# Optimization experiments

Hardware: AMD Instinct MI355X
Metric: run time of the kernel (lower is better)

## Reference

```python
import jax, jax.numpy as jnp
import numpy as np

B, L, D = 2, 2048, 2048
H, G, HD = 16, 4, 128
EPS = 1e-6
THETA_BASE = 10000.0


def setup_inputs() -> dict:
    key = jax.random.key(0)
    ks = jax.random.split(key, 5)
    x = jax.random.normal(ks[0], (B, L, D), jnp.float32)
    Wq = jax.random.normal(ks[1], (D, H * HD), jnp.float32) * 0.02
    Wk = jax.random.normal(ks[2], (D, G * HD), jnp.float32) * 0.02
    Wv = jax.random.normal(ks[3], (D, G * HD), jnp.float32) * 0.02
    Wo = jax.random.normal(ks[4], (H * HD, D), jnp.float32) * 0.02
    q_scale = jnp.ones((HD,), jnp.float32)
    k_scale = jnp.ones((HD,), jnp.float32)
    # Well-formed RoPE tables of shape [L, HD] (duplicated-half layout expected by apply_rope)
    inv_freq = 1.0 / (THETA_BASE ** (jnp.arange(0, HD // 2, dtype=jnp.float32) * 2.0 / HD))  # [HD/2]
    angles = jnp.arange(L, dtype=jnp.float32)[:, None] * inv_freq[None, :]  # [L, HD/2]
    angles = jnp.concatenate([angles, angles], axis=1)  # [L, HD]
    cos = jnp.cos(angles)
    sin = jnp.sin(angles)
    # Causal mask: True = masked (matches masked_fill(mask, -inf))
    mask = jnp.triu(jnp.ones((L, L), dtype=bool), k=1)
    return {"x": x, "Wq": Wq, "Wk": Wk, "Wv": Wv, "Wo": Wo,
            "q_scale": q_scale, "k_scale": k_scale, "cos": cos, "sin": sin, "mask": mask}


def _rmsnorm(x, scale):
    var = jnp.mean(x * x, axis=-1, keepdims=True)
    return x * jax.lax.rsqrt(var + EPS) * scale


def _rope(x, cos, sin):
    # x: [B, h, L, HD]; cos/sin: [L, HD]
    hd = x.shape[-1]
    x1, x2 = x[..., : hd // 2], x[..., hd // 2 :]
    rotated = jnp.concatenate([-x2, x1], axis=-1)
    return x * cos[None, None] + rotated * sin[None, None]


def reference(x, Wq, Wk, Wv, Wo, q_scale, k_scale, cos, sin, mask):
    b, l, _ = x.shape
    q = (x @ Wq).reshape(b, l, H, HD).transpose(0, 2, 1, 3)  # [B,H,L,HD]
    k = (x @ Wk).reshape(b, l, G, HD).transpose(0, 2, 1, 3)  # [B,G,L,HD]
    v = (x @ Wv).reshape(b, l, G, HD).transpose(0, 2, 1, 3)
    q = _rmsnorm(q, q_scale)
    k = _rmsnorm(k, k_scale)
    q = _rope(q, cos, sin)
    k = _rope(k, cos, sin)
    gs = H // G
    k = jnp.repeat(k, gs, axis=1)  # [B,H,L,HD]
    v = jnp.repeat(v, gs, axis=1)
    scores = jnp.einsum('bhqd,bhkd->bhqk', q, k)
    scores = jnp.where(mask, -jnp.inf, scores)
    # NB: faithful to the source's unusual scaling by head_dim**2 (not sqrt)
    w = jax.nn.softmax(scores / float(HD ** 2), axis=-1)
    out = jnp.einsum('bhqk,bhkd->bhqd', w, v).transpose(0, 2, 1, 3).reshape(b, l, H * HD)
    return out @ Wo
```

## Files before the change

kernel.cpp:

```cpp
#include <hip/hip_runtime.h>
#include <math.h>

#define SEQ 2048
#define DMODEL 2048
#define NHQ 16
#define NHK 4

typedef __attribute__((ext_vector_type(8))) short short8;
typedef __attribute__((ext_vector_type(8))) unsigned short ushort8;
typedef __attribute__((ext_vector_type(4))) float floatx4;

__device__ __forceinline__ unsigned short f2bf(float f) {
  unsigned int u = __builtin_bit_cast(unsigned int, f);
  u += 0x7fffu + ((u >> 16) & 1u);
  return (unsigned short)(u >> 16);
}
__device__ __forceinline__ float bf2f(unsigned short s) {
  unsigned int u = ((unsigned int)s) << 16;
  return __builtin_bit_cast(float, u);
}

__global__ __launch_bounds__(256) void prep(const float* __restrict__ x,
                                            const float* __restrict__ Wq,
                                            const float* __restrict__ Wk,
                                            const float* __restrict__ Wv,
                                            const float* __restrict__ Wo,
                                            unsigned short* __restrict__ x_bf,
                                            unsigned short* __restrict__ wqkv_t,
                                            unsigned short* __restrict__ wo_t) {
  const int z = blockIdx.z;
  const int tx = threadIdx.x, ty = threadIdx.y;
  const int tid = ty * 32 + tx;
  if (z == 3) {
    const size_t base = ((size_t)(blockIdx.y * 64 + blockIdx.x)) * 4096 + (size_t)tid * 16;
    const float4 v0 = *(const float4*)(x + base);
    const float4 v1 = *(const float4*)(x + base + 4);
    const float4 v2 = *(const float4*)(x + base + 8);
    const float4 v3 = *(const float4*)(x + base + 12);
    ushort8 w0, w1;
    w0[0] = f2bf(v0.x); w0[1] = f2bf(v0.y); w0[2] = f2bf(v0.z); w0[3] = f2bf(v0.w);
    w0[4] = f2bf(v1.x); w0[5] = f2bf(v1.y); w0[6] = f2bf(v1.z); w0[7] = f2bf(v1.w);
    w1[0] = f2bf(v2.x); w1[1] = f2bf(v2.y); w1[2] = f2bf(v2.z); w1[3] = f2bf(v2.w);
    w1[4] = f2bf(v3.x); w1[5] = f2bf(v3.y); w1[6] = f2bf(v3.z); w1[7] = f2bf(v3.w);
    *(ushort8*)(x_bf + base) = w0;
    *(ushort8*)(x_bf + base + 8) = w1;
    return;
  }
  int bx = blockIdx.x;
  const float* in;
  unsigned short* out;
  int C;
  const int R = 2048;
  if (z == 0)      { in = Wq; out = wqkv_t;                          C = 2048; }
  else if (z == 1) { in = Wo; out = wo_t;                            C = 2048; }
  else {
    if (bx < 16)      { in = Wk; out = wqkv_t + (size_t)2048 * 2048; C = 512; }
    else if (bx < 32) { in = Wv; out = wqkv_t + (size_t)2560 * 2048; C = 512; bx -= 16; }
    else return;
  }
  __shared__ float tile[32][65];
  const int c0 = bx * 32, r0 = blockIdx.y * 64;
#pragma unroll
  for (int j = 0; j < 8; ++j)
    tile[tx][ty + j * 8] = in[(size_t)(r0 + ty + j * 8) * C + c0 + tx];
  __syncthreads();
  const int c = tid >> 3;
  const int l8 = tid & 7;
  ushort8 w;
#pragma unroll
  for (int u = 0; u < 8; ++u) w[u] = f2bf(tile[c][l8 * 8 + u]);
  *(ushort8*)(out + (size_t)(c0 + c) * R + r0 + l8 * 8) = w;
}

__device__ __forceinline__ void stage_tile4(const unsigned short* __restrict__ A,
                                            const unsigned short* __restrict__ Bt,
                                            unsigned short* As, unsigned short* Bs,
                                            int bm, int bn, int K, int k0,
                                            int wave, int srow, int scol) {
#pragma unroll
  for (int it = 0; it < 2; ++it) {
    const int rowa = wave * 32 + it * 16;
    const unsigned short* ga = A + (size_t)(bm + rowa + srow) * K + k0 + scol;
    const unsigned short* gb = Bt + (size_t)(bn + rowa + srow) * K + k0 + scol;
    __builtin_amdgcn_global_load_lds(
        (const __attribute__((address_space(1))) void*)ga,
        (__attribute__((address_space(3))) void*)&As[rowa * 32], 16, 0, 0);
    __builtin_amdgcn_global_load_lds(
        (const __attribute__((address_space(1))) void*)gb,
        (__attribute__((address_space(3))) void*)&Bs[rowa * 32], 16, 0, 0);
  }
}

__device__ __forceinline__ void mfma_tile4(const unsigned short* As, const unsigned short* Bs,
                                           floatx4 (&acc)[4][4],
                                           int wr, int wc, int m15, int quad) {
  const int co = ((quad ^ ((m15 >> 1) & 3)) * 8);
  short8 af[4], bfr[4];
  const unsigned short* pa = &As[(wr * 64 + m15) * 32 + co];
  const unsigned short* pb = &Bs[(wc * 64 + m15) * 32 + co];
#pragma unroll
  for (int i = 0; i < 4; ++i) af[i] = *(const short8*)(pa + i * 16 * 32);
#pragma unroll
  for (int j = 0; j < 4; ++j) bfr[j] = *(const short8*)(pb + j * 16 * 32);
#pragma unroll
  for (int i = 0; i < 4; ++i)
#pragma unroll
    for (int j = 0; j < 4; ++j)
      acc[i][j] = __builtin_amdgcn_mfma_f32_16x16x32_bf16(af[i], bfr[j], acc[i][j], 0, 0, 0);
}

__global__ __launch_bounds__(256) void gemm_qkv_fused(const unsigned short* __restrict__ A,
                                                      const unsigned short* __restrict__ Bt,
                                                      unsigned short* __restrict__ qout,
                                                      unsigned short* __restrict__ kout,
                                                      unsigned short* __restrict__ vout,
                                                      const float* __restrict__ q_scale,
                                                      const float* __restrict__ k_scale,
                                                      const float* __restrict__ cosb,
                                                      const float* __restrict__ sinb) {
  __shared__ unsigned short smem[128 * 129];
  unsigned short* As0 = smem;
  unsigned short* Bs0 = smem + 4096;
  unsigned short* As1 = smem + 8192;
  unsigned short* Bs1 = smem + 12288;

  const int tid = threadIdx.x;
  const int wave = tid >> 6;
  const int lane = tid & 63;
  const int bm = blockIdx.y * 128;
  const int bx = blockIdx.x;
  const int bn = bx * 128;
  const int wr = wave >> 1;
  const int wc = wave & 1;
  const int m15 = lane & 15;
  const int quad = lane >> 4;

  floatx4 acc[4][4];
#pragma unroll
  for (int i = 0; i < 4; ++i)
#pragma unroll
    for (int j = 0; j < 4; ++j) acc[i][j] = (floatx4){0.f, 0.f, 0.f, 0.f};

  const int srow = lane >> 2;
  const int scol = (((lane & 3) ^ ((lane >> 3) & 3))) * 8;

  stage_tile4(A, Bt, As0, Bs0, bm, bn, 2048, 0, wave, srow, scol);
  __syncthreads();

  for (int k0 = 0; k0 < 2048; k0 += 64) {
    stage_tile4(A, Bt, As1, Bs1, bm, bn, 2048, k0 + 32, wave, srow, scol);
    mfma_tile4(As0, Bs0, acc, wr, wc, m15, quad);
    __syncthreads();
    if (k0 + 64 < 2048)
      stage_tile4(A, Bt, As0, Bs0, bm, bn, 2048, k0 + 64, wave, srow, scol);
    mfma_tile4(As1, Bs1, acc, wr, wc, m15, quad);
    __syncthreads();
  }

#pragma unroll
  for (int i = 0; i < 4; ++i)
#pragma unroll
    for (int j = 0; j < 4; ++j) {
      const int col = wc * 64 + j * 16 + m15;
#pragma unroll
      for (int reg = 0; reg < 4; ++reg) {
        const int row = wr * 64 + i * 16 + quad * 4 + reg;
        smem[row * 129 + col] = f2bf(acc[i][j][reg]);
      }
    }
  __syncthreads();

  const int t = tid & 63;
  const int wv = tid >> 6;
  const int b = bm >> 11;
  const int l_base = bm & (SEQ - 1);

  if (bx < 20) {
    const float* scale = (bx < NHQ) ? q_scale : k_scale;
    unsigned short* dstbase = (bx < NHQ)
        ? qout + ((size_t)(b * NHQ + bx) * SEQ + l_base) * 128
        : kout + ((size_t)(b * NHK + (bx - NHQ)) * SEQ + l_base) * 128;
    const float sc0 = scale[t];
    const float sc1 = scale[t + 64];
#pragma unroll 4
    for (int rr = 0; rr < 32; ++rr) {
      const int row = wv * 32 + rr;
      const float v0 = bf2f(smem[row * 129 + t]);
      const float v1 = bf2f(smem[row * 129 + t + 64]);
      float ss = v0 * v0 + v1 * v1;
#pragma unroll
      for (int m = 1; m < 64; m <<= 1) ss += __shfl_xor(ss, m);
      const float r = rsqrtf(ss * (1.0f / 128.0f) + 1e-6f);
      const int l = l_base + row;
      const float c0 = cosb[(size_t)l * 128 + t];
      const float s0 = sinb[(size_t)l * 128 + t];
      const float c1 = cosb[(size_t)l * 128 + t + 64];
      const float s1 = sinb[(size_t)l * 128 + t + 64];
      const float a0 = v0 * r * sc0;
      const float a1 = v1 * r * sc1;
      unsigned short* dst = dstbase + (size_t)row * 128;
      dst[t]      = f2bf(a0 * c0 - a1 * s0);
      dst[t + 64] = f2bf(a1 * c1 + a0 * s1);
    }
  } else {
    const int g = bx - 20;
    unsigned short* vbase = vout + (size_t)(b * NHK + g) * 128 * SEQ + l_base;
#pragma unroll 4
    for (int dd = 0; dd < 32; ++dd) {
      const int d = wv * 32 + dd;
      unsigned short* dst = vbase + (size_t)d * SEQ;
      dst[t]      = smem[t * 129 + d];
      dst[t + 64] = smem[(t + 64) * 129 + d];
    }
  }
}

__global__ __launch_bounds__(256) void gemm_bf16_f32(const unsigned short* __restrict__ A,
                                                     const unsigned short* __restrict__ Bt,
                                                     float* __restrict__ C,
                                                     int M, int N, int K) {
  __shared__ unsigned short smem[4 * 128 * 32];
  unsigned short* As0 = smem;
  unsigned short* Bs0 = smem + 4096;
  unsigned short* As1 = smem + 8192;
  unsigned short* Bs1 = smem + 12288;

  const int tid = threadIdx.x;
  const int wave = tid >> 6;
  const int lane = tid & 63;
  const int bm = blockIdx.y * 128;
  const int bn = blockIdx.x * 128;
  const int wr = wave >> 1;
  const int wc = wave & 1;
  const int m15 = lane & 15;
  const int quad = lane >> 4;

  floatx4 acc[4][4];
#pragma unroll
  for (int i = 0; i < 4; ++i)
#pragma unroll
    for (int j = 0; j < 4; ++j) acc[i][j] = (floatx4){0.f, 0.f, 0.f, 0.f};

  const int srow = lane >> 2;
  const int scol = (((lane & 3) ^ ((lane >> 3) & 3))) * 8;

  stage_tile4(A, Bt, As0, Bs0, bm, bn, K, 0, wave, srow, scol);
  __syncthreads();

  for (int k0 = 0; k0 < K; k0 += 64) {
    stage_tile4(A, Bt, As1, Bs1, bm, bn, K, k0 + 32, wave, srow, scol);
    mfma_tile4(As0, Bs0, acc, wr, wc, m15, quad);
    __syncthreads();
    if (k0 + 64 < K)
      stage_tile4(A, Bt, As0, Bs0, bm, bn, K, k0 + 64, wave, srow, scol);
    mfma_tile4(As1, Bs1, acc, wr, wc, m15, quad);
    __syncthreads();
  }

#pragma unroll
  for (int i = 0; i < 4; ++i)
#pragma unroll
    for (int j = 0; j < 4; ++j) {
      const int col = bn + wc * 64 + j * 16 + m15;
#pragma unroll
      for (int reg = 0; reg < 4; ++reg) {
        const int row = bm + wr * 64 + i * 16 + quad * 4 + reg;
        C[(size_t)row * N + col] = acc[i][j][reg];
      }
    }
}

__global__ __launch_bounds__(256, 4) void attn_mfma(const unsigned short* __restrict__ qb,
                                                    const unsigned short* __restrict__ kb,
                                                    const unsigned short* __restrict__ vtb,
                                                    unsigned short* __restrict__ o) {
  __shared__ unsigned short Ks[64 * 128];
  __shared__ unsigned short Vs[128 * 64];
  unsigned short* Ps = Ks;

  const int tid = threadIdx.x;
  const int wave = tid >> 6;
  const int lane = tid & 63;
  const int m15 = lane & 15;
  const int quad = lane >> 4;
  const int bh = blockIdx.x;
  const int b = bh >> 4;
  const int h = bh & 15;
  const int g = h >> 2;
  const int q0 = ((int)gridDim.y - 1 - (int)blockIdx.y) * 64;

  const unsigned short* qhead = qb + (size_t)bh * SEQ * 128;
  const unsigned short* khead = kb + (size_t)(b * NHK + g) * SEQ * 128;
  const unsigned short* vthead = vtb + (size_t)(b * NHK + g) * 128 * SEQ;

  short8 qf[4];
  {
    const unsigned short* qp = qhead + (size_t)(q0 + wave * 16 + m15) * 128 + quad * 8;
#pragma unroll
    for (int ks = 0; ks < 4; ++ks) qf[ks] = *(const short8*)(qp + ks * 32);
  }

  floatx4 acc_o[8];
#pragma unroll
  for (int n = 0; n < 8; ++n) acc_o[n] = (floatx4){0.f, 0.f, 0.f, 0.f};
  float l_lane[4] = {0.f, 0.f, 0.f, 0.f};
  const float inv_scale = 1.0f / 16384.0f;

  for (int j0 = 0; j0 <= q0; j0 += 64) {
#pragma unroll
    for (int t = 0; t < 4; ++t) {
      const int r = wave * 16 + t * 4 + (lane >> 4);
      const int cg = (lane & 15) ^ (r & 15);
      const unsigned short* src = khead + (size_t)(j0 + r) * 128 + cg * 8;
      __builtin_amdgcn_global_load_lds(
          (const __attribute__((address_space(1))) void*)src,
          (__attribute__((address_space(3))) void*)&Ks[(wave * 16 + t * 4) * 128], 16, 0, 0);
    }
#pragma unroll
    for (int t = 0; t < 4; ++t) {
      const int d = wave * 32 + t * 8 + (lane >> 3);
      const int cg = (lane & 7) ^ (d & 7);
      const unsigned short* src = vthead + (size_t)d * SEQ + j0 + cg * 8;
      __builtin_amdgcn_global_load_lds(
          (const __attribute__((address_space(1))) void*)src,
          (__attribute__((address_space(3))) void*)&Vs[(wave * 32 + t * 8) * 64], 16, 0, 0);
    }
    __syncthreads();

    floatx4 acc_s[4];
#pragma unroll
    for (int n = 0; n < 4; ++n) acc_s[n] = (floatx4){0.f, 0.f, 0.f, 0.f};
#pragma unroll
    for (int ks = 0; ks < 4; ++ks) {
#pragma unroll
      for (int n = 0; n < 4; ++n) {
        const short8 bfrag = *(const short8*)&Ks[(n * 16 + m15) * 128 + (((ks * 4 + quad) ^ m15) * 8)];
        acc_s[n] = __builtin_amdgcn_mfma_f32_16x16x32_bf16(qf[ks], bfrag, acc_s[n], 0, 0, 0);
      }
    }
    __syncthreads();

    if (j0 == q0) {
      const int row_g = wave * 16 + quad * 4;
#pragma unroll
      for (int n = 0; n < 4; ++n) {
        const int col = n * 16 + m15;
#pragma unroll
        for (int rg = 0; rg < 4; ++rg) {
          float p = (col > row_g + rg) ? 0.0f : __expf(acc_s[n][rg] * inv_scale);
          l_lane[rg] += p;
          Ps[(wave * 16 + quad * 4 + rg) * 72 + n * 16 + m15] = f2bf(p);
        }
      }
    } else {
#pragma unroll
      for (int n = 0; n < 4; ++n) {
#pragma unroll
        for (int rg = 0; rg < 4; ++rg) {
          const float p = __expf(acc_s[n][rg] * inv_scale);
          l_lane[rg] += p;
          Ps[(wave * 16 + quad * 4 + rg) * 72 + n * 16 + m15] = f2bf(p);
        }
      }
    }

#pragma unroll
    for (int kk = 0; kk < 2; ++kk) {
      const short8 a = *(const short8*)&Ps[(wave * 16 + m15) * 72 + kk * 32 + quad * 8];
#pragma unroll
      for (int n = 0; n < 8; ++n) {
        const short8 bfrag = *(const short8*)&Vs[(n * 16 + m15) * 64 + (((kk * 4 + quad) ^ (m15 & 7)) * 8)];
        acc_o[n] = __builtin_amdgcn_mfma_f32_16x16x32_bf16(a, bfrag, acc_o[n], 0, 0, 0);
      }
    }
    __syncthreads();
  }

#pragma unroll
  for (int rg = 0; rg < 4; ++rg) {
    float l = l_lane[rg];
    l += __shfl_xor(l, 1);
    l += __shfl_xor(l, 2);
    l += __shfl_xor(l, 4);
    l += __shfl_xor(l, 8);
    const float invl = 1.0f / l;
    const size_t row = (size_t)(b * SEQ + q0 + wave * 16 + quad * 4 + rg);
#pragma unroll
    for (int n = 0; n < 8; ++n)
      o[row * DMODEL + h * 128 + n * 16 + m15] = f2bf(acc_o[n][rg] * invl);
  }
}

extern "C" void kernel_launch(void* const* d_in, const int* in_sizes, int n_in,
                              void* d_out, int out_size, void* d_ws, size_t ws_size,
                              hipStream_t stream) {
  const float* x       = (const float*)d_in[0];
  const float* Wq      = (const float*)d_in[1];
  const float* Wk      = (const float*)d_in[2];
  const float* Wv      = (const float*)d_in[3];
  const float* Wo      = (const float*)d_in[4];
  const float* q_scale = (const float*)d_in[5];
  const float* k_scale = (const float*)d_in[6];
  const float* cosb    = (const float*)d_in[7];
  const float* sinb    = (const float*)d_in[8];
  float* out = (float*)d_out;

  char* w = (char*)d_ws;
  unsigned short* x_bf    = (unsigned short*)w;
  unsigned short* wqkv_t  = (unsigned short*)(w + 16777216);
  unsigned short* q_bf    = (unsigned short*)(w + 29360128);
  unsigned short* k_bf    = (unsigned short*)(w + 46137344);
  unsigned short* vt      = (unsigned short*)(w + 50331648);
  unsigned short* wo_t    = (unsigned short*)(w + 54525952);
  unsigned short* attn_bf = (unsigned short*)(w + 62914560);

  prep<<<dim3(64, 32, 4), dim3(32, 8), 0, stream>>>(x, Wq, Wk, Wv, Wo, x_bf, wqkv_t, wo_t);

  gemm_qkv_fused<<<dim3(24, 32), 256, 0, stream>>>(x_bf, wqkv_t, q_bf, k_bf, vt,
                                                   q_scale, k_scale, cosb, sinb);

  attn_mfma<<<dim3(2 * NHQ, SEQ / 64), 256, 0, stream>>>(q_bf, k_bf, vt, attn_bf);
  gemm_bf16_f32<<<dim3(2048 / 128, 4096 / 128), 256, 0, stream>>>(
      attn_bf, wo_t, out, 4096, 2048, 2048);
}
```

Measured before the change: 312.8 us.

## Triple-buffer GEMM K-loop staging with partial vmcnt waits and one barrier

Both the fused QKV GEMM and the output-projection GEMM move from a two-buffer LDS ping-pong to a rotating three-buffer pipeline that prefetches two K-slices ahead. Each iteration now waits only for the oldest outstanding global loads (vmcnt(4)) instead of draining them all, and uses a single raw s_barrier with a scheduling fence. The aim is to hide more global-load latency behind the MFMA work and cut barrier stalls per K step. In exchange the LDS footprint per block grows, which can lower occupancy. Correctness also depends on the hand-written vmcnt count matching how many loads stage_tile4 issues.

```diff
diff --git a/kernel.cpp b/kernel.cpp
--- a/kernel.cpp
+++ b/kernel.cpp
@@ -109,6 +109,14 @@
       acc[i][j] = __builtin_amdgcn_mfma_f32_16x16x32_bf16(af[i], bfr[j], acc[i][j], 0, 0, 0);
 }
 
+#define KLOOP_SYNC(cond_deep)                                   \
+  do {                                                          \
+    if (cond_deep) asm volatile("s_waitcnt vmcnt(4)" ::: "memory"); \
+    else           asm volatile("s_waitcnt vmcnt(0)" ::: "memory"); \
+    __builtin_amdgcn_s_barrier();                               \
+    __builtin_amdgcn_sched_barrier(0);                          \
+  } while (0)
+
 __global__ __launch_bounds__(256) void gemm_qkv_fused(const unsigned short* __restrict__ A,
                                                       const unsigned short* __restrict__ Bt,
                                                       unsigned short* __restrict__ qout,
@@ -118,11 +126,7 @@
                                                       const float* __restrict__ k_scale,
                                                       const float* __restrict__ cosb,
                                                       const float* __restrict__ sinb) {
-  __shared__ unsigned short smem[128 * 129];
-  unsigned short* As0 = smem;
-  unsigned short* Bs0 = smem + 4096;
-  unsigned short* As1 = smem + 8192;
-  unsigned short* Bs1 = smem + 12288;
+  __shared__ unsigned short smem[3 * 8192];
 
   const int tid = threadIdx.x;
   const int wave = tid >> 6;
@@ -144,17 +148,21 @@
   const int srow = lane >> 2;
   const int scol = (((lane & 3) ^ ((lane >> 3) & 3))) * 8;
 
-  stage_tile4(A, Bt, As0, Bs0, bm, bn, 2048, 0, wave, srow, scol);
-  __syncthreads();
-
-  for (int k0 = 0; k0 < 2048; k0 += 64) {
-    stage_tile4(A, Bt, As1, Bs1, bm, bn, 2048, k0 + 32, wave, srow, scol);
-    mfma_tile4(As0, Bs0, acc, wr, wc, m15, quad);
-    __syncthreads();
-    if (k0 + 64 < 2048)
-      stage_tile4(A, Bt, As0, Bs0, bm, bn, 2048, k0 + 64, wave, srow, scol);
-    mfma_tile4(As1, Bs1, acc, wr, wc, m15, quad);
-    __syncthreads();
+  unsigned short* c0 = smem;
+  unsigned short* c1 = smem + 8192;
+  unsigned short* c2 = smem + 16384;
+
+  stage_tile4(A, Bt, c0, c0 + 4096, bm, bn, 2048, 0, wave, srow, scol);
+  stage_tile4(A, Bt, c1, c1 + 4096, bm, bn, 2048, 32, wave, srow, scol);
+  KLOOP_SYNC(true);
+
+  const int NK = 64;
+  for (int t = 0; t < NK; ++t) {
+    if (t + 2 < NK)
+      stage_tile4(A, Bt, c2, c2 + 4096, bm, bn, 2048, (t + 2) * 32, wave, srow, scol);
+    mfma_tile4(c0, c0 + 4096, acc, wr, wc, m15, quad);
+    KLOOP_SYNC(t + 2 < NK);
+    unsigned short* tmp = c0; c0 = c1; c1 = c2; c2 = tmp;
   }
 
 #pragma unroll
@@ -192,15 +200,15 @@
       for (int m = 1; m < 64; m <<= 1) ss += __shfl_xor(ss, m);
       const float r = rsqrtf(ss * (1.0f / 128.0f) + 1e-6f);
       const int l = l_base + row;
-      const float c0 = cosb[(size_t)l * 128 + t];
+      const float c0v = cosb[(size_t)l * 128 + t];
       const float s0 = sinb[(size_t)l * 128 + t];
-      const float c1 = cosb[(size_t)l * 128 + t + 64];
+      const float c1v = cosb[(size_t)l * 128 + t + 64];
       const float s1 = sinb[(size_t)l * 128 + t + 64];
       const float a0 = v0 * r * sc0;
       const float a1 = v1 * r * sc1;
       unsigned short* dst = dstbase + (size_t)row * 128;
-      dst[t]      = f2bf(a0 * c0 - a1 * s0);
-      dst[t + 64] = f2bf(a1 * c1 + a0 * s1);
+      dst[t]      = f2bf(a0 * c0v - a1 * s0);
+      dst[t + 64] = f2bf(a1 * c1v + a0 * s1);
     }
   } else {
     const int g = bx - 20;
@@ -219,11 +227,7 @@
                                                      const unsigned short* __restrict__ Bt,
                                                      float* __restrict__ C,
                                                      int M, int N, int K) {
-  __shared__ unsigned short smem[4 * 128 * 32];
-  unsigned short* As0 = smem;
-  unsigned short* Bs0 = smem + 4096;
-  unsigned short* As1 = smem + 8192;
-  unsigned short* Bs1 = smem + 12288;
+  __shared__ unsigned short smem[3 * 8192];
 
   const int tid = threadIdx.x;
   const int wave = tid >> 6;
@@ -244,17 +248,21 @@
   const int srow = lane >> 2;
   const int scol = (((lane & 3) ^ ((lane >> 3) & 3))) * 8;
 
-  stage_tile4(A, Bt, As0, Bs0, bm, bn, K, 0, wave, srow, scol);
-  __syncthreads();
-
-  for (int k0 = 0; k0 < K; k0 += 64) {
-    stage_tile4(A, Bt, As1, Bs1, bm, bn, K, k0 + 32, wave, srow, scol);
-    mfma_tile4(As0, Bs0, acc, wr, wc, m15, quad);
-    __syncthreads();
-    if (k0 + 64 < K)
-      stage_tile4(A, Bt, As0, Bs0, bm, bn, K, k0 + 64, wave, srow, scol);
-    mfma_tile4(As1, Bs1, acc, wr, wc, m15, quad);
-    __syncthreads();
+  unsigned short* c0 = smem;
+  unsigned short* c1 = smem + 8192;
+  unsigned short* c2 = smem + 16384;
+
+  stage_tile4(A, Bt, c0, c0 + 4096, bm, bn, K, 0, wave, srow, scol);
+  stage_tile4(A, Bt, c1, c1 + 4096, bm, bn, K, 32, wave, srow, scol);
+  KLOOP_SYNC(true);
+
+  const int NK = K >> 5;
+  for (int t = 0; t < NK; ++t) {
+    if (t + 2 < NK)
+      stage_tile4(A, Bt, c2, c2 + 4096, bm, bn, K, (t + 2) * 32, wave, srow, scol);
+    mfma_tile4(c0, c0 + 4096, acc, wr, wc, m15, quad);
+    KLOOP_SYNC(t + 2 < NK);
+    unsigned short* tmp = c0; c0 = c1; c1 = c2; c2 = tmp;
   }
 
 #pragma unroll
```

Result: faster. 305.1 us (-2.5%).
